# Optimization experiments

Measured on AMD Instinct MI355X. Metric: run time of the kernel, lower is better.

Reference implementation:

```python
import jax, jax.numpy as jnp
import numpy as np

Q = 9          # D2Q9
G = 8          # dihedral group of the square
X = YD = 768   # spatial grid
HID = 32       # tau_net hidden width
N_IN = 6       # moments with order <= 2 (indices 0..5, contiguous by construction)
LOWER_TAU = 0.8


def _build_stencil():
    # D2Q9 velocities and weights
    e = np.array([[0, 0], [1, 0], [0, 1], [-1, 0], [0, -1],
                  [1, 1], [-1, 1], [-1, -1], [1, -1]], dtype=np.float64)
    w = np.array([4 / 9] + [1 / 9] * 4 + [1 / 36] * 4, dtype=np.float64)
    # natural moment matrix: rows are monomials ex^px * ey^py, ordered so that
    # moment_order = [0,1,1,2,2,2,3,3,4]  ->  in_indices=[0..5], out_indices=[6,7,8]
    exps = [(0, 0), (1, 0), (0, 1), (2, 0), (1, 1), (0, 2), (2, 1), (1, 2), (2, 2)]
    M = np.stack([e[:, 0] ** px * e[:, 1] ** py for px, py in exps])  # [Q, Q]
    Minv = np.linalg.inv(M)
    # symmetry group of the square: 4 rotations x {id, x-axis reflection}
    rots = [np.array([[np.cos(a), -np.sin(a)], [np.sin(a), np.cos(a)]])
            for a in (0.0, np.pi / 2, np.pi, 3 * np.pi / 2)]
    refl = np.array([[1.0, 0.0], [0.0, -1.0]])
    Rs = rots + [r @ refl for r in rots]
    perms = []
    for R in Rs:
        Re = np.rint(e @ R.T)
        P = np.zeros((Q, Q))
        for i in range(Q):
            j = int(np.where((e == Re[i]).all(axis=1))[0][0])
            P[j, i] = 1.0  # velocity i maps to velocity j under R
        perms.append(P)
    P = np.stack(perms)                                   # [G, Q, Q]
    actions = np.einsum('qp,gpr,rs->gqs', M, P, Minv)      # moment action  M P M^-1
    Pt = P.transpose(0, 2, 1)                              # P^-1 = P^T
    inv_actions = np.einsum('qp,gpr,rs->gqs', M, Pt, Minv)
    return (M.astype(np.float32), Minv.astype(np.float32),
            actions.astype(np.float32), inv_actions.astype(np.float32),
            e.astype(np.float32), w.astype(np.float32))


def setup_inputs() -> dict:
    key = jax.random.key(0)
    kf, k1, k2, k3 = jax.random.split(key, 4)
    M, Minv, actions, inv_actions, e, w = _build_stencil()
    f = jax.random.uniform(kf, (Q, X, YD), dtype=jnp.float32)
    s = 0.1
    return {
        'f': f,
        'M': jnp.asarray(M), 'Minv': jnp.asarray(Minv),
        'actions': jnp.asarray(actions), 'inv_actions': jnp.asarray(inv_actions),
        'e': jnp.asarray(e), 'w': jnp.asarray(w),
        'W1': jax.random.normal(k1, (N_IN, HID), jnp.float32) * s,
        'b1': jnp.zeros((HID,), jnp.float32),
        'W2': jax.random.normal(k2, (HID, HID), jnp.float32) * s,
        'b2': jnp.zeros((HID,), jnp.float32),
        'W3': jax.random.normal(k3, (HID, Q - N_IN), jnp.float32) * s,
        'b3': jnp.zeros((Q - N_IN,), jnp.float32),
    }


def reference(f, M, Minv, actions, inv_actions, e, w, W1, b1, W2, b2, W3, b3):
    # --- moment transform: m = M f, moved to channel-last [X, Y, Q] ---
    m = jnp.einsum('qp,pxy->xyq', M, f)
    # --- equivariant tau net on low-order moments ---
    x_in = m[..., :N_IN]                                   # in_indices = 0..5
    Ainv = inv_actions[:, :N_IN, :N_IN]                    # [G, 6, 6]
    A = actions[:, N_IN:, N_IN:]                           # [G, 3, 3] (out_indices)
    xg = jnp.einsum('gij,xyj->gxyi', Ainv, x_in)           # [G, X, Y, 6]
    h = jax.nn.relu(xg @ W1 + b1)
    h = jax.nn.relu(h @ W2 + b2)
    o = h @ W3 + b3                                        # [G, X, Y, 3]
    out = jnp.einsum('gij,gxyj->xyi', A, o)                # sum over group -> [X, Y, 3]
    tau_hi = 1.5 + jax.nn.elu(out)                         # gt_half: > 0.5
    taus = jnp.full(m.shape, LOWER_TAU, m.dtype).at[..., N_IN:].set(tau_hi)
    # --- equilibrium moments: meq = M feq(rho, u) (quadratic BGK, cs^2=1/3) ---
    rho = m[..., 0:1]                                      # natural moments: m0=rho
    u = m[..., 1:3] / rho                                  # m1,m2 = momentum
    eu = jnp.einsum('qd,xyd->xyq', e, u)
    usq = jnp.sum(u * u, axis=-1, keepdims=True)
    feq = w * rho * (1.0 + 3.0 * eu + 4.5 * eu * eu - 1.5 * usq)
    meq = jnp.einsum('qp,xyp->xyq', M, feq)
    # --- MRT collision + inverse transform ---
    m_post = m - (m - meq) / taus
    return jnp.einsum('pq,xyq->pxy', Minv, m_post)
```

## Files before the change

### kernel.cpp

```cpp
#include <hip/hip_runtime.h>
#include <math.h>

#define Q 9
#define NPIX (768 * 768)

typedef short bf16x8 __attribute__((ext_vector_type(8)));
typedef float f32x4 __attribute__((ext_vector_type(4)));
typedef int i32x4 __attribute__((ext_vector_type(4)));

#define A1BV 512
#define A3V  1024
#define A2V  1536
#define B3TF 6656

__device__ __forceinline__ unsigned short f2bf(float x) {
    unsigned u = __builtin_bit_cast(unsigned, x);
    unsigned r = u + 0x7FFFu + ((u >> 16) & 1u);
    return (unsigned short)(r >> 16);
}

__device__ __forceinline__ unsigned packrnd(float e, float o) {
    unsigned ue = __builtin_bit_cast(unsigned, e) + 0x8000u;
    unsigned uo = __builtin_bit_cast(unsigned, o) + 0x8000u;
    return (uo & 0xFFFF0000u) | (ue >> 16);
}

__device__ __forceinline__ bf16x8 mk8(unsigned w0, unsigned w1, unsigned w2, unsigned w3) {
    i32x4 t = {(int)w0, (int)w1, (int)w2, (int)w3};
    return __builtin_bit_cast(bf16x8, t);
}

__global__ void prep_kernel(const float* __restrict__ actions,
                            const float* __restrict__ inv_actions,
                            const float* __restrict__ W1,
                            const float* __restrict__ b1,
                            const float* __restrict__ W2,
                            const float* __restrict__ W3,
                            const float* __restrict__ b3,
                            short* __restrict__ wsb,
                            float* __restrict__ wsf) {
    const int t = threadIdx.x;
    for (int idx = t; idx < 8192; idx += 256) {
        int j = idx & 7, l = (idx >> 3) & 63, g = (idx >> 9) & 7, half = idx >> 12;
        int m = l & 15, quad = l >> 4, k = quad * 8 + j;
        int feat = 8 * (m >> 2) + (m & 3) + 4 * half;
        float v = 0.f;
        if (k < 6) {
            for (int i = 0; i < 6; i++)
                v += inv_actions[g * 81 + i * 9 + k] * W1[i * 32 + feat];
        } else if (k == 6) v = b1[feat];
        wsb[idx] = (short)f2bf(v);
    }
    for (int idx = t; idx < 4096; idx += 256) {
        int j = idx & 7, l = (idx >> 3) & 63, g = idx >> 9;
        int m = l & 15, quad = l >> 4, k = quad * 8 + j;
        float v = 0.f;
        if (m < 3)
            for (int j3 = 0; j3 < 3; j3++)
                v += W3[k * 3 + j3] * actions[g * 81 + (6 + m) * 9 + (6 + j3)];
        wsb[8192 + idx] = (short)f2bf(v);
    }
    for (int idx = t; idx < 1024; idx += 256) {
        int j = idx & 7, l = (idx >> 3) & 63, half = idx >> 9;
        int m = l & 15, quad = l >> 4, k = quad * 8 + j;
        int feat = 8 * (m >> 2) + (m & 3) + 4 * half;
        wsb[12288 + idx] = (short)f2bf(W2[k * 32 + feat]);
    }
    if (t < 3) {
        float acc = 0.f;
        for (int g = 0; g < 8; g++)
            for (int j = 0; j < 3; j++)
                acc += actions[g * 81 + (6 + t) * 9 + (6 + j)] * b3[j];
        wsf[B3TF + t] = acc;
    }
}

__global__ __launch_bounds__(256, 4) void lbm_kernel(
    const float* __restrict__ f,
    const float* __restrict__ Minv,
    const float* __restrict__ w,
    const float* __restrict__ b2,
    const short* __restrict__ wsb,
    const float* __restrict__ wsf,
    float* __restrict__ out) {
    __shared__ float oL[4][64][4];

    const int tid = threadIdx.x;
    const int wv = tid >> 6;
    const int l = tid & 63;
    const int quad = l >> 4;
    const int lc = l & 15;
    const int p = blockIdx.x * 256 + tid;

    float fv0 = f[0 * NPIX + p], fv1 = f[1 * NPIX + p], fv2 = f[2 * NPIX + p];
    float fv3 = f[3 * NPIX + p], fv4 = f[4 * NPIX + p], fv5 = f[5 * NPIX + p];
    float fv6 = f[6 * NPIX + p], fv7 = f[7 * NPIX + p], fv8 = f[8 * NPIX + p];
    float sa = fv5 + fv6, sb = fv7 + fv8, sc = fv5 - fv6, sd = fv7 - fv8;
    float sab = sa + sb;
    float m8 = sab, m6 = sa - sb, m4 = sc + sd, m7 = sc - sd;
    float p13 = fv1 + fv3, d13 = fv1 - fv3, p24 = fv2 + fv4, d24 = fv2 - fv4;
    float m0 = fv0 + p13 + p24 + sab;
    float m1 = d13 + m7;
    float m2 = d24 + m6;
    float m3 = p13 + sab;
    float m5 = p24 + sab;

    unsigned mp0 = packrnd(m0, m1), mp1 = packrnd(m2, m3), mp2 = packrnd(m4, m5);
    const unsigned CONE = 0x00003F80u;
    bf16x8 B1[4];
    #pragma unroll
    for (int nb = 0; nb < 4; nb++) {
        int src = ((nb << 4) | lc) << 2;
        unsigned a = (unsigned)__builtin_amdgcn_ds_bpermute(src, (int)mp0);
        unsigned b = (unsigned)__builtin_amdgcn_ds_bpermute(src, (int)mp1);
        unsigned c = (unsigned)__builtin_amdgcn_ds_bpermute(src, (int)mp2);
        B1[nb] = mk8(a, b, c, CONE);
    }

    const bf16x8* wsv = (const bf16x8*)wsb;
    bf16x8 a2a = wsv[A2V + l], a2b = wsv[A2V + 64 + l];
    f32x4 c2iA = *(const f32x4*)(b2 + 8 * quad);
    f32x4 c2iB = *(const f32x4*)(b2 + 8 * quad + 4);
    float b30 = wsf[B3TF + 0], b31 = wsf[B3TF + 1], b32 = wsf[B3TF + 2];
    f32x4 oinit;
    oinit[0] = (quad == 0) ? b30 : 0.f;
    oinit[1] = (quad == 0) ? b31 : 0.f;
    oinit[2] = (quad == 0) ? b32 : 0.f;
    oinit[3] = 0.f;
    f32x4 oacc[4] = {oinit, oinit, oinit, oinit};

    bf16x8 a1a = wsv[l], a1b = wsv[A1BV + l], a3 = wsv[A3V + l];

    #pragma unroll 1
    for (int g = 0; g < 8; g++) {
        const int gn = (g + 1) & 7;
        bf16x8 na1a = wsv[gn * 64 + l];
        bf16x8 na1b = wsv[A1BV + gn * 64 + l];
        bf16x8 na3  = wsv[A3V + gn * 64 + l];
        #pragma unroll
        for (int nb = 0; nb < 4; nb++) {
            f32x4 z = {0.f, 0.f, 0.f, 0.f};
            f32x4 c1a = __builtin_amdgcn_mfma_f32_16x16x32_bf16(a1a, B1[nb], z, 0, 0, 0);
            f32x4 c1b = __builtin_amdgcn_mfma_f32_16x16x32_bf16(a1b, B1[nb], z, 0, 0, 0);
            bf16x8 B2 = mk8(
                packrnd(fmaxf(c1a[0], 0.f), fmaxf(c1a[1], 0.f)),
                packrnd(fmaxf(c1a[2], 0.f), fmaxf(c1a[3], 0.f)),
                packrnd(fmaxf(c1b[0], 0.f), fmaxf(c1b[1], 0.f)),
                packrnd(fmaxf(c1b[2], 0.f), fmaxf(c1b[3], 0.f)));
            f32x4 c2a = __builtin_amdgcn_mfma_f32_16x16x32_bf16(a2a, B2, c2iA, 0, 0, 0);
            f32x4 c2b = __builtin_amdgcn_mfma_f32_16x16x32_bf16(a2b, B2, c2iB, 0, 0, 0);
            bf16x8 B3 = mk8(
                packrnd(fmaxf(c2a[0], 0.f), fmaxf(c2a[1], 0.f)),
                packrnd(fmaxf(c2a[2], 0.f), fmaxf(c2a[3], 0.f)),
                packrnd(fmaxf(c2b[0], 0.f), fmaxf(c2b[1], 0.f)),
                packrnd(fmaxf(c2b[2], 0.f), fmaxf(c2b[3], 0.f)));
            oacc[nb] = __builtin_amdgcn_mfma_f32_16x16x32_bf16(a3, B3, oacc[nb], 0, 0, 0);
        }
        a1a = na1a; a1b = na1b; a3 = na3;
    }

    if (quad == 0) {
        #pragma unroll
        for (int nb = 0; nb < 4; nb++)
            *(f32x4*)&oL[wv][nb * 16 + lc][0] = oacc[nb];
    }
    f32x4 ov = *(const f32x4*)&oL[wv][l][0];
    float o_[3] = {ov[0], ov[1], ov[2]};

    float tinv[3];
    #pragma unroll
    for (int i = 0; i < 3; i++) {
        float o = o_[i];
        float el = (o > 0.f) ? o : (__expf(o) - 1.f);
        tinv[i] = 1.f / (1.5f + el);
    }

    float rho = m0;
    float ir = 1.f / rho;
    float ux = m1 * ir, uy = m2 * ir;
    float usq = ux * ux + uy * uy;
    float base = 1.f - 1.5f * usq;
    float w0r = w[0] * rho, w1r = w[1] * rho, w5r = w[5] * rho;
    float feq0 = w0r * base;
    float ax = 4.5f * ux * ux + base, bx = 3.f * ux;
    float feq1 = w1r * (ax + bx), feq3 = w1r * (ax - bx);
    float ay = 4.5f * uy * uy + base, by = 3.f * uy;
    float feq2 = w1r * (ay + by), feq4 = w1r * (ay - by);
    float ss = ux + uy, as_ = 4.5f * ss * ss + base, bs = 3.f * ss;
    float feq5 = w5r * (as_ + bs), feq7 = w5r * (as_ - bs);
    float dd = uy - ux, ad = 4.5f * dd * dd + base, bd = 3.f * dd;
    float feq6 = w5r * (ad + bd), feq8 = w5r * (ad - bd);

    float ea = feq5 + feq6, eb = feq7 + feq8, ec = feq5 - feq6, ed = feq7 - feq8;
    float eab = ea + eb;
    float q8 = eab, q6 = ea - eb, q4 = ec + ed, q7 = ec - ed;
    float ep13 = feq1 + feq3, ed13 = feq1 - feq3, ep24 = feq2 + feq4, ed24 = feq2 - feq4;
    float q0 = feq0 + ep13 + ep24 + eab;
    float q1 = ed13 + q7, q2 = ed24 + q6, q3 = ep13 + eab, q5 = ep24 + eab;

    float mp_[9];
    mp_[0] = m0 - (m0 - q0) * 1.25f;
    mp_[1] = m1 - (m1 - q1) * 1.25f;
    mp_[2] = m2 - (m2 - q2) * 1.25f;
    mp_[3] = m3 - (m3 - q3) * 1.25f;
    mp_[4] = m4 - (m4 - q4) * 1.25f;
    mp_[5] = m5 - (m5 - q5) * 1.25f;
    mp_[6] = m6 - (m6 - q6) * tinv[0];
    mp_[7] = m7 - (m7 - q7) * tinv[1];
    mp_[8] = m8 - (m8 - q8) * tinv[2];

    #pragma unroll
    for (int q = 0; q < 9; q++) {
        float acc = Minv[q * 9 + 0] * mp_[0];
        #pragma unroll
        for (int pp = 1; pp < 9; pp++) acc = fmaf(Minv[q * 9 + pp], mp_[pp], acc);
        __builtin_nontemporal_store(acc, &out[q * NPIX + p]);
    }
}

extern "C" void kernel_launch(void* const* d_in, const int* in_sizes, int n_in,
                              void* d_out, int out_size, void* d_ws, size_t ws_size,
                              hipStream_t stream) {
    const float* f           = (const float*)d_in[0];
    const float* Minv        = (const float*)d_in[2];
    const float* actions     = (const float*)d_in[3];
    const float* inv_actions = (const float*)d_in[4];
    const float* w           = (const float*)d_in[6];
    const float* W1          = (const float*)d_in[7];
    const float* b1          = (const float*)d_in[8];
    const float* W2          = (const float*)d_in[9];
    const float* b2          = (const float*)d_in[10];
    const float* W3          = (const float*)d_in[11];
    const float* b3          = (const float*)d_in[12];
    float* outp = (float*)d_out;
    short* wsb = (short*)d_ws;
    float* wsf = (float*)d_ws;

    prep_kernel<<<1, 256, 0, stream>>>(actions, inv_actions, W1, b1, W2, W3, b3, wsb, wsf);
    lbm_kernel<<<NPIX / 256, 256, 0, stream>>>(f, Minv, w, b2, wsb, wsf, outp);
}
```

Measured before the change: 147.0 us.

## Parallelize weight prep across blocks and use hardware bf16 pack and rcp

The weight-preparation kernel runs on 53 blocks with one element per thread instead of a single block looping, which shortens the serial prologue before the main kernel. The manual bf16 rounding pack is replaced by the HIP float2-to-bfloat162 conversion, which may map to a packed convert instruction on this hardware. Two divisions become hardware reciprocal approximations, trading a little accuracy for fewer instructions.

```diff
diff --git a/kernel.cpp b/kernel.cpp
--- a/kernel.cpp
+++ b/kernel.cpp
@@ -1,4 +1,5 @@
 #include <hip/hip_runtime.h>
+#include <hip/hip_bf16.h>
 #include <math.h>
 
 #define Q 9
@@ -19,10 +20,11 @@
     return (unsigned short)(r >> 16);
 }
 
-__device__ __forceinline__ unsigned packrnd(float e, float o) {
-    unsigned ue = __builtin_bit_cast(unsigned, e) + 0x8000u;
-    unsigned uo = __builtin_bit_cast(unsigned, o) + 0x8000u;
-    return (uo & 0xFFFF0000u) | (ue >> 16);
+__device__ __forceinline__ unsigned pk2(float e, float o) {
+    __hip_bfloat162 h = __float22bfloat162_rn(make_float2(e, o));
+    unsigned u;
+    __builtin_memcpy(&u, &h, 4);
+    return u;
 }
 
 __device__ __forceinline__ bf16x8 mk8(unsigned w0, unsigned w1, unsigned w2, unsigned w3) {
@@ -39,36 +41,40 @@
                             const float* __restrict__ b3,
                             short* __restrict__ wsb,
                             float* __restrict__ wsf) {
-    const int t = threadIdx.x;
-    for (int idx = t; idx < 8192; idx += 256) {
+    const int idx = blockIdx.x * 256 + threadIdx.x;
+    if (idx < 8192) {
         int j = idx & 7, l = (idx >> 3) & 63, g = (idx >> 9) & 7, half = idx >> 12;
         int m = l & 15, quad = l >> 4, k = quad * 8 + j;
         int feat = 8 * (m >> 2) + (m & 3) + 4 * half;
         float v = 0.f;
         if (k < 6) {
+            #pragma unroll
             for (int i = 0; i < 6; i++)
                 v += inv_actions[g * 81 + i * 9 + k] * W1[i * 32 + feat];
         } else if (k == 6) v = b1[feat];
         wsb[idx] = (short)f2bf(v);
-    }
-    for (int idx = t; idx < 4096; idx += 256) {
-        int j = idx & 7, l = (idx >> 3) & 63, g = idx >> 9;
+    } else if (idx < 12288) {
+        int t = idx - 8192;
+        int j = t & 7, l = (t >> 3) & 63, g = t >> 9;
         int m = l & 15, quad = l >> 4, k = quad * 8 + j;
         float v = 0.f;
-        if (m < 3)
+        if (m < 3) {
+            #pragma unroll
             for (int j3 = 0; j3 < 3; j3++)
                 v += W3[k * 3 + j3] * actions[g * 81 + (6 + m) * 9 + (6 + j3)];
-        wsb[8192 + idx] = (short)f2bf(v);
-    }
-    for (int idx = t; idx < 1024; idx += 256) {
-        int j = idx & 7, l = (idx >> 3) & 63, half = idx >> 9;
+        }
+        wsb[idx] = (short)f2bf(v);
+    } else if (idx < 13312) {
+        int t = idx - 12288;
+        int j = t & 7, l = (t >> 3) & 63, half = t >> 9;
         int m = l & 15, quad = l >> 4, k = quad * 8 + j;
         int feat = 8 * (m >> 2) + (m & 3) + 4 * half;
-        wsb[12288 + idx] = (short)f2bf(W2[k * 32 + feat]);
-    }
-    if (t < 3) {
+        wsb[idx] = (short)f2bf(W2[k * 32 + feat]);
+    } else if (idx < 13315) {
+        int t = idx - 13312;
         float acc = 0.f;
         for (int g = 0; g < 8; g++)
+            #pragma unroll
             for (int j = 0; j < 3; j++)
                 acc += actions[g * 81 + (6 + t) * 9 + (6 + j)] * b3[j];
         wsf[B3TF + t] = acc;
@@ -105,7 +111,7 @@
     float m3 = p13 + sab;
     float m5 = p24 + sab;
 
-    unsigned mp0 = packrnd(m0, m1), mp1 = packrnd(m2, m3), mp2 = packrnd(m4, m5);
+    unsigned mp0 = pk2(m0, m1), mp1 = pk2(m2, m3), mp2 = pk2(m4, m5);
     const unsigned CONE = 0x00003F80u;
     bf16x8 B1[4];
     #pragma unroll
@@ -143,17 +149,17 @@
             f32x4 c1a = __builtin_amdgcn_mfma_f32_16x16x32_bf16(a1a, B1[nb], z, 0, 0, 0);
             f32x4 c1b = __builtin_amdgcn_mfma_f32_16x16x32_bf16(a1b, B1[nb], z, 0, 0, 0);
             bf16x8 B2 = mk8(
-                packrnd(fmaxf(c1a[0], 0.f), fmaxf(c1a[1], 0.f)),
-                packrnd(fmaxf(c1a[2], 0.f), fmaxf(c1a[3], 0.f)),
-                packrnd(fmaxf(c1b[0], 0.f), fmaxf(c1b[1], 0.f)),
-                packrnd(fmaxf(c1b[2], 0.f), fmaxf(c1b[3], 0.f)));
+                pk2(fmaxf(c1a[0], 0.f), fmaxf(c1a[1], 0.f)),
+                pk2(fmaxf(c1a[2], 0.f), fmaxf(c1a[3], 0.f)),
+                pk2(fmaxf(c1b[0], 0.f), fmaxf(c1b[1], 0.f)),
+                pk2(fmaxf(c1b[2], 0.f), fmaxf(c1b[3], 0.f)));
             f32x4 c2a = __builtin_amdgcn_mfma_f32_16x16x32_bf16(a2a, B2, c2iA, 0, 0, 0);
             f32x4 c2b = __builtin_amdgcn_mfma_f32_16x16x32_bf16(a2b, B2, c2iB, 0, 0, 0);
             bf16x8 B3 = mk8(
-                packrnd(fmaxf(c2a[0], 0.f), fmaxf(c2a[1], 0.f)),
-                packrnd(fmaxf(c2a[2], 0.f), fmaxf(c2a[3], 0.f)),
-                packrnd(fmaxf(c2b[0], 0.f), fmaxf(c2b[1], 0.f)),
-                packrnd(fmaxf(c2b[2], 0.f), fmaxf(c2b[3], 0.f)));
+                pk2(fmaxf(c2a[0], 0.f), fmaxf(c2a[1], 0.f)),
+                pk2(fmaxf(c2a[2], 0.f), fmaxf(c2a[3], 0.f)),
+                pk2(fmaxf(c2b[0], 0.f), fmaxf(c2b[1], 0.f)),
+                pk2(fmaxf(c2b[2], 0.f), fmaxf(c2b[3], 0.f)));
             oacc[nb] = __builtin_amdgcn_mfma_f32_16x16x32_bf16(a3, B3, oacc[nb], 0, 0, 0);
         }
         a1a = na1a; a1b = na1b; a3 = na3;
@@ -172,11 +178,11 @@
     for (int i = 0; i < 3; i++) {
         float o = o_[i];
         float el = (o > 0.f) ? o : (__expf(o) - 1.f);
-        tinv[i] = 1.f / (1.5f + el);
+        tinv[i] = __builtin_amdgcn_rcpf(1.5f + el);
     }
 
     float rho = m0;
-    float ir = 1.f / rho;
+    float ir = __builtin_amdgcn_rcpf(rho);
     float ux = m1 * ir, uy = m2 * ir;
     float usq = ux * ux + uy * uy;
     float base = 1.f - 1.5f * usq;
@@ -236,6 +242,6 @@
     short* wsb = (short*)d_ws;
     float* wsf = (float*)d_ws;
 
-    prep_kernel<<<1, 256, 0, stream>>>(actions, inv_actions, W1, b1, W2, W3, b3, wsb, wsf);
+    prep_kernel<<<53, 256, 0, stream>>>(actions, inv_actions, W1, b1, W2, W3, b3, wsb, wsf);
     lbm_kernel<<<NPIX / 256, 256, 0, stream>>>(f, Minv, w, b2, wsb, wsf, outp);
 }
```

Result: faster. 135.4 us (-7.9%).
